# Kernel tuning notes

Hardware: AMD Instinct MI355X
Metric: run time of the kernel (lower is better)

## Reference

```python
import jax, jax.numpy as jnp
import numpy as np

IN_DIM, OUT_DIM = 256, 64
N_D, N_G, N_C, N_S = 100000, 50000, 50000, 20000
E = 1000000
ALPHA = 0.2  # LeakyReLU negative slope


def setup_inputs() -> dict:
    key = jax.random.key(0)
    ks = jax.random.split(key, 14)
    scale = float(np.sqrt(6.0 / (IN_DIM + OUT_DIM)) * 1.414)
    scale_w = float(np.sqrt(6.0 / (4 * OUT_DIM + OUT_DIM)) * 1.414)
    return {
        "disease_feats": jax.random.normal(ks[0], (N_D, IN_DIM), jnp.float32),
        "gene_feats": jax.random.normal(ks[1], (N_G, IN_DIM), jnp.float32),
        "chemical_feats": jax.random.normal(ks[2], (N_C, IN_DIM), jnp.float32),
        "species_feats": jax.random.normal(ks[3], (N_S, IN_DIM), jnp.float32),
        "P_disease": jax.random.uniform(ks[4], (IN_DIM, OUT_DIM), jnp.float32, -scale, scale),
        "P_gene": jax.random.uniform(ks[5], (IN_DIM, OUT_DIM), jnp.float32, -scale, scale),
        "P_chemical": jax.random.uniform(ks[6], (IN_DIM, OUT_DIM), jnp.float32, -scale, scale),
        "P_species": jax.random.uniform(ks[7], (IN_DIM, OUT_DIM), jnp.float32, -scale, scale),
        "W_GDCD": jax.random.uniform(ks[8], (4 * OUT_DIM, OUT_DIM), jnp.float32, -scale_w, scale_w),
        "idx_d0": jax.random.randint(ks[9], (E,), 0, N_D, jnp.int32),
        "idx_d1": jax.random.randint(ks[10], (E,), 0, N_D, jnp.int32),
        "idx_g": jax.random.randint(ks[11], (E,), 0, N_G, jnp.int32),
        "idx_c": jax.random.randint(ks[12], (E,), 0, N_C, jnp.int32),
    }


def reference(disease_feats, gene_feats, chemical_feats, species_feats,
              P_disease, P_gene, P_chemical, P_species, W_GDCD,
              idx_d0, idx_d1, idx_g, idx_c):
    # Per-type linear projections (pattern 'GDCD')
    f_disease = disease_feats @ P_disease      # [N_D, out]
    f_gene = gene_feats @ P_gene               # [N_G, out]
    f_chemical = chemical_feats @ P_chemical   # [N_C, out]
    # f_species is computed by the torch code but unused for GDCD; omitted (dead code under jit)
    # Gather per-instance rows and concat -> [E, 4*out]
    concat = jnp.concatenate(
        [f_disease[idx_d0], f_disease[idx_d1], f_gene[idx_g], f_chemical[idx_c]], axis=1)
    instance = concat @ W_GDCD                 # [E, out]
    return jax.nn.leaky_relu(instance, negative_slope=ALPHA)
```

## Files before the change

### kernel.cpp

```cpp
#include <hip/hip_runtime.h>

typedef __attribute__((ext_vector_type(8))) short          short8;
typedef __attribute__((ext_vector_type(4))) float          f32x4;
typedef __attribute__((ext_vector_type(8))) unsigned short ushort8;

#define ALPHA 0.2f

__device__ __forceinline__ unsigned short f2bf(float f) {
    union { float f; unsigned int u; } x; x.f = f;
    unsigned int u = x.u;
    u += 0x7fffu + ((u >> 16) & 1u);
    return (unsigned short)(u >> 16);
}
__device__ __forceinline__ float bf2f(unsigned short u) {
    union { unsigned int i; float f; } x; x.i = ((unsigned int)u) << 16;
    return x.f;
}

__global__ __launch_bounds__(256)
void make_frags(const float* __restrict__ Pd, const float* __restrict__ Pg,
                const float* __restrict__ Pc, const float* __restrict__ W,
                unsigned short* __restrict__ fd, unsigned short* __restrict__ fg,
                unsigned short* __restrict__ fc) {
    int t = blockIdx.x * 256 + threadIdx.x;
    int local, NCT, mbase; unsigned short* dst;
    if (t < 32768)      { local = t;         NCT = 8; dst = fd; mbase = 0; }
    else if (t < 49152) { local = t - 32768; NCT = 4; dst = fg; mbase = 2; }
    else                { local = t - 49152; NCT = 4; dst = fc; mbase = 3; }
    int j    = local & 7;
    int lane = (local >> 3) & 63;
    int ct   = (local >> 9) & (NCT - 1);
    int kk   = local >> (9 + (NCT == 8 ? 3 : 2));
    int k = kk * 32 + ((lane >> 4) << 3) + j;
    int c = ct * 16 + (lane & 15);
    int m, cc; const float* P;
    if (NCT == 8) { m = (c < 64) ? 0 : 1; cc = c & 63; P = Pd; }
    else          { m = mbase;            cc = c;      P = (mbase == 2) ? Pg : Pc; }
    float acc = 0.f;
    #pragma unroll 8
    for (int q = 0; q < 64; ++q)
        acc += P[k * 64 + q] * W[(m * 64 + q) * 64 + cc];
    dst[local] = f2bf(acc);
}

template <int NCT>
__device__ __forceinline__
void proj_body(const float* __restrict__ feats,
               const unsigned short* __restrict__ bfrag,
               unsigned short* __restrict__ g, int ntiles, int blk,
               unsigned short* blds) {
    const int t = threadIdx.x;
    #pragma unroll
    for (int i = 0; i < NCT * 2; ++i) {
        int off = (i * 512 + t) * 8;
        *(int4*)&blds[off] = *(const int4*)&bfrag[off];
    }
    __syncthreads();

    const int wid = t >> 6, lane = t & 63;
    const int C = NCT * 16;
    const int tile = blk * 8 + wid;
    if (tile >= ntiles) return;

    const int row = tile * 16 + (lane & 15);
    const float* arow = feats + (size_t)row * 256 + ((lane >> 4) * 8);

    f32x4 acc[NCT];
    #pragma unroll
    for (int ct = 0; ct < NCT; ++ct) acc[ct] = (f32x4){0.f, 0.f, 0.f, 0.f};

    #pragma unroll
    for (int kk = 0; kk < 8; ++kk) {
        f32x4 v0 = *(const f32x4*)(arow + kk * 32);
        f32x4 v1 = *(const f32x4*)(arow + kk * 32 + 4);
        short8 a;
        a[0] = (short)f2bf(v0[0]); a[1] = (short)f2bf(v0[1]);
        a[2] = (short)f2bf(v0[2]); a[3] = (short)f2bf(v0[3]);
        a[4] = (short)f2bf(v1[0]); a[5] = (short)f2bf(v1[1]);
        a[6] = (short)f2bf(v1[2]); a[7] = (short)f2bf(v1[3]);
        #pragma unroll
        for (int ct = 0; ct < NCT; ++ct) {
            short8 b = *(const short8*)&blds[((kk * NCT + ct) * 64 + lane) * 8];
            acc[ct] = __builtin_amdgcn_mfma_f32_16x16x32_bf16(a, b, acc[ct], 0, 0, 0);
        }
    }

    const int rbase = tile * 16 + (lane >> 4) * 4;
    const int cbase = lane & 15;
    #pragma unroll
    for (int ct = 0; ct < NCT; ++ct) {
        #pragma unroll
        for (int j = 0; j < 4; ++j)
            g[(size_t)(rbase + j) * C + ct * 16 + cbase] = f2bf(acc[ct][j]);
    }
}

__global__ __launch_bounds__(512)
void proj_all(const float* __restrict__ featd, const float* __restrict__ featg,
              const float* __restrict__ featc,
              const unsigned short* __restrict__ fragd,
              const unsigned short* __restrict__ fragg,
              const unsigned short* __restrict__ fragc,
              unsigned short* __restrict__ g_d, unsigned short* __restrict__ g_g,
              unsigned short* __restrict__ g_c,
              int nbd, int nbg, int td, int tg, int tc) {
    __shared__ unsigned short blds[32768];
    int b = blockIdx.x;
    if (b < nbd)            proj_body<8>(featd, fragd, g_d, td, b,             blds);
    else if (b < nbd + nbg) proj_body<4>(featg, fragg, g_g, tg, b - nbd,       blds);
    else                    proj_body<4>(featc, fragc, g_c, tc, b - nbd - nbg, blds);
}

__global__ __launch_bounds__(256)
void gather_kernel(const unsigned short* __restrict__ g_d,
                   const unsigned short* __restrict__ g_g,
                   const unsigned short* __restrict__ g_c,
                   const int* __restrict__ i0, const int* __restrict__ i1,
                   const int* __restrict__ ig, const int* __restrict__ ic,
                   float* __restrict__ out, int E) {
    int tid = blockIdx.x * 256 + threadIdx.x;
    int e = tid >> 3;
    if (e >= E) return;
    int q = tid & 7;

    int a  = __builtin_nontemporal_load(i0 + e);
    int b  = __builtin_nontemporal_load(i1 + e);
    int gi = __builtin_nontemporal_load(ig + e);
    int ci = __builtin_nontemporal_load(ic + e);

    ushort8 v0 = *(const ushort8*)(g_d + (size_t)a * 128 + q * 8);
    ushort8 v1 = *(const ushort8*)(g_d + (size_t)b * 128 + 64 + q * 8);
    ushort8 v2 = *(const ushort8*)(g_g + (size_t)gi * 64 + q * 8);
    ushort8 v3 = *(const ushort8*)(g_c + (size_t)ci * 64 + q * 8);

    f32x4 r0, r1;
    #pragma unroll
    for (int j = 0; j < 4; ++j) {
        float s = bf2f(v0[j]) + bf2f(v1[j]) + bf2f(v2[j]) + bf2f(v3[j]);
        r0[j] = s >= 0.f ? s : s * ALPHA;
    }
    #pragma unroll
    for (int j = 0; j < 4; ++j) {
        float s = bf2f(v0[j + 4]) + bf2f(v1[j + 4]) + bf2f(v2[j + 4]) + bf2f(v3[j + 4]);
        r1[j] = s >= 0.f ? s : s * ALPHA;
    }

    float* o = out + (size_t)e * 64 + q * 8;
    __builtin_nontemporal_store(r0, (f32x4*)o);
    __builtin_nontemporal_store(r1, (f32x4*)(o + 4));
}

extern "C" void kernel_launch(void* const* d_in, const int* in_sizes, int n_in,
                              void* d_out, int out_size, void* d_ws, size_t ws_size,
                              hipStream_t stream) {
    const float* feats_d = (const float*)d_in[0];
    const float* feats_g = (const float*)d_in[1];
    const float* feats_c = (const float*)d_in[2];
    const float* Pd = (const float*)d_in[4];
    const float* Pg = (const float*)d_in[5];
    const float* Pc = (const float*)d_in[6];
    const float* W  = (const float*)d_in[8];
    const int* i0 = (const int*)d_in[9];
    const int* i1 = (const int*)d_in[10];
    const int* ig = (const int*)d_in[11];
    const int* ic = (const int*)d_in[12];
    float* out = (float*)d_out;

    const int N_D = in_sizes[0] / 256;
    const int N_G = in_sizes[1] / 256;
    const int N_C = in_sizes[2] / 256;
    const int E   = in_sizes[9];

    char* ws = (char*)d_ws;
    unsigned short* fd  = (unsigned short*)ws;
    unsigned short* fg  = (unsigned short*)(ws + 65536);
    unsigned short* fc  = (unsigned short*)(ws + 98304);
    unsigned short* g_d = (unsigned short*)(ws + 131072);
    unsigned short* g_g = g_d + (size_t)N_D * 128;
    unsigned short* g_c = g_g + (size_t)N_G * 64;

    make_frags<<<256, 256, 0, stream>>>(Pd, Pg, Pc, W, fd, fg, fc);

    int td = N_D / 16, tg = N_G / 16, tc = N_C / 16;
    int nbd = (td + 7) / 8, nbg = (tg + 7) / 8, nbc = (tc + 7) / 8;
    proj_all<<<nbd + nbg + nbc, 512, 0, stream>>>(
        feats_d, feats_g, feats_c, fd, fg, fc, g_d, g_g, g_c,
        nbd, nbg, td, tg, tc);

    long long nthreads = (long long)E * 8;
    gather_kernel<<<(int)((nthreads + 255) / 256), 256, 0, stream>>>(
        g_d, g_g, g_c, i0, i1, ig, ic, out, E);
}
```

Before: 168.5 us.

## Process two tiles per wave in projection and two edges per gather thread

The projection kernel now has each wave handle two 16-row tiles, so each block loads its LDS weight fragments once for twice the rows. Feature reads now use nontemporal loads. The LDS fragment copy loop is cut to NCT iterations, which matches the fragment size; the old loop copied twice as much and ran past the buffers. The gather kernel now has each thread process edges e and e+E/2, issuing both sets of index and row loads before computing, for more memory-level parallelism, at the cost of more registers and half as many threads.

```diff
diff --git a/kernel.cpp b/kernel.cpp
--- a/kernel.cpp
+++ b/kernel.cpp
@@ -43,6 +43,8 @@
     dst[local] = f2bf(acc);
 }
 
+#define TPW 2
+
 template <int NCT>
 __device__ __forceinline__
 void proj_body(const float* __restrict__ feats,
@@ -51,7 +53,7 @@
                unsigned short* blds) {
     const int t = threadIdx.x;
     #pragma unroll
-    for (int i = 0; i < NCT * 2; ++i) {
+    for (int i = 0; i < NCT; ++i) {
         int off = (i * 512 + t) * 8;
         *(int4*)&blds[off] = *(const int4*)&bfrag[off];
     }
@@ -59,39 +61,43 @@
 
     const int wid = t >> 6, lane = t & 63;
     const int C = NCT * 16;
-    const int tile = blk * 8 + wid;
-    if (tile >= ntiles) return;
-
-    const int row = tile * 16 + (lane & 15);
-    const float* arow = feats + (size_t)row * 256 + ((lane >> 4) * 8);
-
-    f32x4 acc[NCT];
+
     #pragma unroll
-    for (int ct = 0; ct < NCT; ++ct) acc[ct] = (f32x4){0.f, 0.f, 0.f, 0.f};
-
-    #pragma unroll
-    for (int kk = 0; kk < 8; ++kk) {
-        f32x4 v0 = *(const f32x4*)(arow + kk * 32);
-        f32x4 v1 = *(const f32x4*)(arow + kk * 32 + 4);
-        short8 a;
-        a[0] = (short)f2bf(v0[0]); a[1] = (short)f2bf(v0[1]);
-        a[2] = (short)f2bf(v0[2]); a[3] = (short)f2bf(v0[3]);
-        a[4] = (short)f2bf(v1[0]); a[5] = (short)f2bf(v1[1]);
-        a[6] = (short)f2bf(v1[2]); a[7] = (short)f2bf(v1[3]);
+    for (int it = 0; it < TPW; ++it) {
+        const int tile = (blk * 8 + wid) * TPW + it;
+        if (tile >= ntiles) return;
+
+        const int row = tile * 16 + (lane & 15);
+        const float* arow = feats + (size_t)row * 256 + ((lane >> 4) * 8);
+
+        f32x4 acc[NCT];
+        #pragma unroll
+        for (int ct = 0; ct < NCT; ++ct) acc[ct] = (f32x4){0.f, 0.f, 0.f, 0.f};
+
+        #pragma unroll
+        for (int kk = 0; kk < 8; ++kk) {
+            f32x4 v0 = __builtin_nontemporal_load((const f32x4*)(arow + kk * 32));
+            f32x4 v1 = __builtin_nontemporal_load((const f32x4*)(arow + kk * 32 + 4));
+            short8 a;
+            a[0] = (short)f2bf(v0[0]); a[1] = (short)f2bf(v0[1]);
+            a[2] = (short)f2bf(v0[2]); a[3] = (short)f2bf(v0[3]);
+            a[4] = (short)f2bf(v1[0]); a[5] = (short)f2bf(v1[1]);
+            a[6] = (short)f2bf(v1[2]); a[7] = (short)f2bf(v1[3]);
+            #pragma unroll
+            for (int ct = 0; ct < NCT; ++ct) {
+                short8 b = *(const short8*)&blds[((kk * NCT + ct) * 64 + lane) * 8];
+                acc[ct] = __builtin_amdgcn_mfma_f32_16x16x32_bf16(a, b, acc[ct], 0, 0, 0);
+            }
+        }
+
+        const int rbase = tile * 16 + (lane >> 4) * 4;
+        const int cbase = lane & 15;
         #pragma unroll
         for (int ct = 0; ct < NCT; ++ct) {
-            short8 b = *(const short8*)&blds[((kk * NCT + ct) * 64 + lane) * 8];
-            acc[ct] = __builtin_amdgcn_mfma_f32_16x16x32_bf16(a, b, acc[ct], 0, 0, 0);
+            #pragma unroll
+            for (int j = 0; j < 4; ++j)
+                g[(size_t)(rbase + j) * C + ct * 16 + cbase] = f2bf(acc[ct][j]);
         }
-    }
-
-    const int rbase = tile * 16 + (lane >> 4) * 4;
-    const int cbase = lane & 15;
-    #pragma unroll
-    for (int ct = 0; ct < NCT; ++ct) {
-        #pragma unroll
-        for (int j = 0; j < 4; ++j)
-            g[(size_t)(rbase + j) * C + ct * 16 + cbase] = f2bf(acc[ct][j]);
     }
 }
 
@@ -117,37 +123,63 @@
                    const unsigned short* __restrict__ g_c,
                    const int* __restrict__ i0, const int* __restrict__ i1,
                    const int* __restrict__ ig, const int* __restrict__ ic,
-                   float* __restrict__ out, int E) {
+                   float* __restrict__ out, int E, int Eh) {
     int tid = blockIdx.x * 256 + threadIdx.x;
-    int e = tid >> 3;
-    if (e >= E) return;
-    int q = tid & 7;
-
-    int a  = __builtin_nontemporal_load(i0 + e);
-    int b  = __builtin_nontemporal_load(i1 + e);
-    int gi = __builtin_nontemporal_load(ig + e);
-    int ci = __builtin_nontemporal_load(ic + e);
-
-    ushort8 v0 = *(const ushort8*)(g_d + (size_t)a * 128 + q * 8);
-    ushort8 v1 = *(const ushort8*)(g_d + (size_t)b * 128 + 64 + q * 8);
-    ushort8 v2 = *(const ushort8*)(g_g + (size_t)gi * 64 + q * 8);
-    ushort8 v3 = *(const ushort8*)(g_c + (size_t)ci * 64 + q * 8);
+    int e0 = tid >> 3;
+    if (e0 >= Eh) return;
+    int q = tid & 3;
+    q = tid & 7;
+    int e1 = e0 + Eh;
+    bool has1 = e1 < E;
+
+    int a0  = __builtin_nontemporal_load(i0 + e0);
+    int b0  = __builtin_nontemporal_load(i1 + e0);
+    int gi0 = __builtin_nontemporal_load(ig + e0);
+    int ci0 = __builtin_nontemporal_load(ic + e0);
+    int a1 = 0, b1 = 0, gi1 = 0, ci1 = 0;
+    if (has1) {
+        a1  = __builtin_nontemporal_load(i0 + e1);
+        b1  = __builtin_nontemporal_load(i1 + e1);
+        gi1 = __builtin_nontemporal_load(ig + e1);
+        ci1 = __builtin_nontemporal_load(ic + e1);
+    }
+
+    ushort8 v0 = *(const ushort8*)(g_d + (size_t)a0  * 128 + q * 8);
+    ushort8 v1 = *(const ushort8*)(g_d + (size_t)b0  * 128 + 64 + q * 8);
+    ushort8 v2 = *(const ushort8*)(g_g + (size_t)gi0 * 64 + q * 8);
+    ushort8 v3 = *(const ushort8*)(g_c + (size_t)ci0 * 64 + q * 8);
+    ushort8 w0, w1, w2, w3;
+    if (has1) {
+        w0 = *(const ushort8*)(g_d + (size_t)a1  * 128 + q * 8);
+        w1 = *(const ushort8*)(g_d + (size_t)b1  * 128 + 64 + q * 8);
+        w2 = *(const ushort8*)(g_g + (size_t)gi1 * 64 + q * 8);
+        w3 = *(const ushort8*)(g_c + (size_t)ci1 * 64 + q * 8);
+    }
 
     f32x4 r0, r1;
     #pragma unroll
     for (int j = 0; j < 4; ++j) {
         float s = bf2f(v0[j]) + bf2f(v1[j]) + bf2f(v2[j]) + bf2f(v3[j]);
         r0[j] = s >= 0.f ? s : s * ALPHA;
-    }
-    #pragma unroll
-    for (int j = 0; j < 4; ++j) {
-        float s = bf2f(v0[j + 4]) + bf2f(v1[j + 4]) + bf2f(v2[j + 4]) + bf2f(v3[j + 4]);
-        r1[j] = s >= 0.f ? s : s * ALPHA;
-    }
-
-    float* o = out + (size_t)e * 64 + q * 8;
-    __builtin_nontemporal_store(r0, (f32x4*)o);
-    __builtin_nontemporal_store(r1, (f32x4*)(o + 4));
+        float u = bf2f(v0[j + 4]) + bf2f(v1[j + 4]) + bf2f(v2[j + 4]) + bf2f(v3[j + 4]);
+        r1[j] = u >= 0.f ? u : u * ALPHA;
+    }
+    float* o0 = out + (size_t)e0 * 64 + q * 8;
+    __builtin_nontemporal_store(r0, (f32x4*)o0);
+    __builtin_nontemporal_store(r1, (f32x4*)(o0 + 4));
+
+    if (has1) {
+        #pragma unroll
+        for (int j = 0; j < 4; ++j) {
+            float s = bf2f(w0[j]) + bf2f(w1[j]) + bf2f(w2[j]) + bf2f(w3[j]);
+            r0[j] = s >= 0.f ? s : s * ALPHA;
+            float u = bf2f(w0[j + 4]) + bf2f(w1[j + 4]) + bf2f(w2[j + 4]) + bf2f(w3[j + 4]);
+            r1[j] = u >= 0.f ? u : u * ALPHA;
+        }
+        float* o1 = out + (size_t)e1 * 64 + q * 8;
+        __builtin_nontemporal_store(r0, (f32x4*)o1);
+        __builtin_nontemporal_store(r1, (f32x4*)(o1 + 4));
+    }
 }
 
 extern "C" void kernel_launch(void* const* d_in, const int* in_sizes, int n_in,
@@ -182,12 +214,15 @@
     make_frags<<<256, 256, 0, stream>>>(Pd, Pg, Pc, W, fd, fg, fc);
 
     int td = N_D / 16, tg = N_G / 16, tc = N_C / 16;
-    int nbd = (td + 7) / 8, nbg = (tg + 7) / 8, nbc = (tc + 7) / 8;
+    int nbd = (td + 8 * TPW - 1) / (8 * TPW);
+    int nbg = (tg + 8 * TPW - 1) / (8 * TPW);
+    int nbc = (tc + 8 * TPW - 1) / (8 * TPW);
     proj_all<<<nbd + nbg + nbc, 512, 0, stream>>>(
         feats_d, feats_g, feats_c, fd, fg, fc, g_d, g_g, g_c,
         nbd, nbg, td, tg, tc);
 
-    long long nthreads = (long long)E * 8;
+    int Eh = (E + 1) / 2;
+    long long nthreads = (long long)Eh * 8;
     gather_kernel<<<(int)((nthreads + 255) / 256), 256, 0, stream>>>(
-        g_d, g_g, g_c, i0, i1, ig, ic, out, E);
-}
+        g_d, g_g, g_c, i0, i1, ig, ic, out, E, Eh);
+}
```

New measurement: 201.5 us. +19.6%, slower.
